# Kernel optimization log

Measured on AMD Instinct MI355X. Metric: run time of the kernel, lower is better.

## Reference

```python
import jax, jax.numpy as jnp
import numpy as np

N, E, D_IN, D_H, D_OUT = 50000, 600000, 128, 128, 1


def setup_inputs() -> dict:
    key = jax.random.key(0)
    ks = jax.random.split(key, 20)
    p = lambda k, sh: jax.random.normal(k, sh, dtype=jnp.float32) * 0.05
    return {
        "x": jax.random.normal(ks[0], (N, D_IN), dtype=jnp.float32),
        "edge_weight": jax.random.uniform(ks[1], (E,), dtype=jnp.float32),
        # input LEConv (lin1: W1/b1, lin2: W2 no bias, lin3: W3/b3)
        "W1_in": p(ks[2], (D_IN, D_H)), "b1_in": jnp.zeros((D_H,), jnp.float32),
        "W2_in": p(ks[3], (D_IN, D_H)),
        "W3_in": p(ks[4], (D_IN, D_H)), "b3_in": jnp.zeros((D_H,), jnp.float32),
        # inner LEConv
        "W1_h": p(ks[5], (D_H, D_H)), "b1_h": jnp.zeros((D_H,), jnp.float32),
        "W2_h": p(ks[6], (D_H, D_H)),
        "W3_h": p(ks[7], (D_H, D_H)), "b3_h": jnp.zeros((D_H,), jnp.float32),
        # output LEConv
        "W1_o": p(ks[8], (D_H, D_OUT)), "b1_o": jnp.zeros((D_OUT,), jnp.float32),
        "W2_o": p(ks[9], (D_H, D_OUT)),
        "W3_o": p(ks[10], (D_H, D_OUT)), "b3_o": jnp.zeros((D_OUT,), jnp.float32),
        # LayerNorms
        "g1": jnp.ones((D_H,), jnp.float32), "beta1": jnp.zeros((D_H,), jnp.float32),
        "g2": jnp.ones((D_H,), jnp.float32), "beta2": jnp.zeros((D_H,), jnp.float32),
        "edge_index": jax.random.randint(ks[11], (2, E), 0, N, dtype=jnp.int32),
        "number_of_layers": 4,
    }


def _leconv(x, src, dst, w, W1, b1, W2, W3, b3):
    # PyG LEConv: out_i = lin3(x_i) + sum_{j->i} w_e * (lin1(x_j) - lin2(x_i))
    a = x @ W1 + b1                                   # [N, D_out]
    b = x @ W2                                        # [N, D_out]
    wsum = jax.ops.segment_sum(w, dst, num_segments=N)             # [N]
    agg = jax.ops.segment_sum(w[:, None] * a[src], dst, num_segments=N)  # [N, D_out]
    return agg - b * wsum[:, None] + x @ W3 + b3


def _ln(x, g, b, eps=1e-5):
    m = x.mean(-1, keepdims=True)
    v = x.var(-1, keepdims=True)
    return (x - m) * jax.lax.rsqrt(v + eps) * g + b


def reference(x, edge_weight, W1_in, b1_in, W2_in, W3_in, b3_in,
              W1_h, b1_h, W2_h, W3_h, b3_h,
              W1_o, b1_o, W2_o, W3_o, b3_o,
              g1, beta1, g2, beta2, edge_index, number_of_layers):
    src, dst = edge_index[0], edge_index[1]
    # per-feature standardization over nodes (torch std is unbiased -> ddof=1)
    x = (x - x.mean(0, keepdims=True)) / (jnp.std(x, axis=0, ddof=1, keepdims=True) + 1e-6)
    h = jax.nn.leaky_relu(
        _ln(_leconv(x, src, dst, edge_weight, W1_in, b1_in, W2_in, W3_in, b3_in), g1, beta1),
        negative_slope=0.1)
    for _ in range(number_of_layers - 2):
        h = jax.nn.leaky_relu(
            _ln(_leconv(h, src, dst, edge_weight, W1_h, b1_h, W2_h, W3_h, b3_h), g2, beta2),
            negative_slope=0.1)
    h = _leconv(h, src, dst, edge_weight, W1_o, b1_o, W2_o, W3_o, b3_o)
    return jax.nn.sigmoid(h)
```

## Files before the change

kernel.cpp:

```cpp
#include <hip/hip_runtime.h>
#include <hip/hip_bf16.h>
#include <math.h>


typedef _Float16 f16x8 __attribute__((ext_vector_type(8)));
typedef _Float16 f16x4 __attribute__((ext_vector_type(4)));
typedef float f32x4 __attribute__((ext_vector_type(4)));

#define LSTRIDE 136

__device__ inline float wave_reduce_sum(float v) {
    #pragma unroll
    for (int off = 32; off > 0; off >>= 1)
        v += __shfl_xor(v, off, 64);
    return v;
}


__global__ __launch_bounds__(256) void hist_kernel(
    const int* __restrict__ dst, int* __restrict__ deg, int E)
{
    int e = blockIdx.x * 256 + threadIdx.x;
    if (e < E) atomicAdd(&deg[dst[e]], 1);
}

__global__ __launch_bounds__(256) void scan_pass1(
    const int* __restrict__ deg, int N, int* __restrict__ partial)
{
    __shared__ int sh[256];
    int t = threadIdx.x;
    int base = blockIdx.x * 1024 + t * 4;
    int s = 0;
    #pragma unroll
    for (int i = 0; i < 4; ++i) { int idx = base + i; if (idx < N) s += deg[idx]; }
    sh[t] = s; __syncthreads();
    for (int off = 128; off > 0; off >>= 1) {
        if (t < off) sh[t] += sh[t + off];
        __syncthreads();
    }
    if (t == 0) partial[blockIdx.x] = sh[0];
}

__global__ __launch_bounds__(256) void scan_pass2(int* __restrict__ partial, int nb)
{
    __shared__ int sh[256];
    int t = threadIdx.x;
    sh[t] = (t < nb) ? partial[t] : 0;
    __syncthreads();
    for (int off = 1; off < 256; off <<= 1) {
        int x = sh[t];
        if (t >= off) x += sh[t - off];
        __syncthreads();
        sh[t] = x;
        __syncthreads();
    }
    if (t < nb) partial[t] = (t > 0) ? sh[t - 1] : 0;
}

__global__ __launch_bounds__(256) void scan_pass3(
    const int* __restrict__ deg, int N, const int* __restrict__ partial,
    int* __restrict__ rowptr, int* __restrict__ fill, int E)
{
    __shared__ int sh[256];
    int t = threadIdx.x;
    int base = blockIdx.x * 1024 + t * 4;
    int v[4]; int s = 0;
    #pragma unroll
    for (int i = 0; i < 4; ++i) { int idx = base + i; v[i] = (idx < N) ? deg[idx] : 0; s += v[i]; }
    sh[t] = s; __syncthreads();
    for (int off = 1; off < 256; off <<= 1) {
        int x = sh[t];
        if (t >= off) x += sh[t - off];
        __syncthreads();
        sh[t] = x;
        __syncthreads();
    }
    int off0 = partial[blockIdx.x] + ((t > 0) ? sh[t - 1] : 0);
    #pragma unroll
    for (int i = 0; i < 4; ++i) {
        int idx = base + i;
        if (idx < N) { rowptr[idx] = off0; fill[idx] = off0; off0 += v[i]; }
    }
    if (blockIdx.x == 0 && t == 0) rowptr[N] = E;
}

__global__ __launch_bounds__(256) void csr_fill_kernel(
    const int* __restrict__ src, const int* __restrict__ dst,
    const float* __restrict__ ew, int* __restrict__ fill,
    int2* __restrict__ csr, int E)
{
    int e = blockIdx.x * 256 + threadIdx.x;
    if (e >= E) return;
    int d = dst[e];
    int pos = atomicAdd(&fill[d], 1);
    csr[pos] = make_int2(src[e], __float_as_int(ew[e]));
}

__global__ __launch_bounds__(256) void wsum_csr_kernel(
    const int* __restrict__ rowptr, const int2* __restrict__ csr,
    float* __restrict__ wsum, int N)
{
    int n = blockIdx.x * 256 + threadIdx.x;
    if (n >= N) return;
    int b = rowptr[n], en = rowptr[n + 1];
    float s = 0.f;
    for (int e = b; e < en; ++e) s += __int_as_float(csr[e].y);
    wsum[n] = s;
}


__global__ __launch_bounds__(256) void convert_weights_kernel(
    const float* __restrict__ W1, const float* __restrict__ W2,
    const float* __restrict__ W3, _Float16* __restrict__ Wt)
{
    int idx = blockIdx.x * 256 + threadIdx.x;
    if (idx >= 384 * 128) return;
    int n = idx >> 7, k = idx & 127;
    const float* W = (n < 128) ? W1 : (n < 256) ? W2 : W3;
    int c = n & 127;
    Wt[idx] = (_Float16)W[k * 128 + c];
}


#define CS_BLOCKS 512

__global__ __launch_bounds__(256) void colstats_kernel(
    const float* __restrict__ x, int N,
    float* __restrict__ ps, float* __restrict__ pss)
{
    __shared__ float shs[256][4];
    __shared__ float shq[256][4];
    int t = threadIdx.x;
    int g = t >> 5;
    int c = t & 31;
    const float4* xv = (const float4*)x;
    float s0=0.f,s1=0.f,s2=0.f,s3=0.f, q0=0.f,q1=0.f,q2=0.f,q3=0.f;
    for (int r = blockIdx.x * 8 + g; r < N; r += CS_BLOCKS * 8) {
        float4 v = xv[(size_t)r * 32 + c];
        s0 += v.x; s1 += v.y; s2 += v.z; s3 += v.w;
        q0 += v.x*v.x; q1 += v.y*v.y; q2 += v.z*v.z; q3 += v.w*v.w;
    }
    shs[t][0]=s0; shs[t][1]=s1; shs[t][2]=s2; shs[t][3]=s3;
    shq[t][0]=q0; shq[t][1]=q1; shq[t][2]=q2; shq[t][3]=q3;
    __syncthreads();
    if (t < 32) {
        float S[4] = {0,0,0,0}, Q[4] = {0,0,0,0};
        #pragma unroll
        for (int gg = 0; gg < 8; ++gg) {
            #pragma unroll
            for (int i = 0; i < 4; ++i) {
                S[i] += shs[t + 32*gg][i];
                Q[i] += shq[t + 32*gg][i];
            }
        }
        #pragma unroll
        for (int i = 0; i < 4; ++i) {
            ps [blockIdx.x * 128 + t*4 + i] = S[i];
            pss[blockIdx.x * 128 + t*4 + i] = Q[i];
        }
    }
}

__global__ __launch_bounds__(256) void reduce_stats_kernel(
    const float* __restrict__ ps, const float* __restrict__ pss, int N,
    float* __restrict__ mean, float* __restrict__ rstd)
{
    __shared__ float sh[256];
    int t = threadIdx.x;
    int f = t & 127;
    const float* src = (t >= 128) ? pss : ps;
    float s = 0.f;
    for (int r = 0; r < CS_BLOCKS; ++r) s += src[r * 128 + f];
    sh[t] = s;
    __syncthreads();
    if (t < 128) {
        float sum = sh[t], sumsq = sh[t + 128];
        float m = sum / (float)N;
        float var = (sumsq - sum * sum / (float)N) / (float)(N - 1);
        var = fmaxf(var, 0.f);
        mean[t] = m;
        rstd[t] = 1.f / (sqrtf(var) + 1e-6f);
    }
}

__global__ __launch_bounds__(256) void standardize_kernel(
    const float* __restrict__ x, const float* __restrict__ mean,
    const float* __restrict__ rstd, _Float16* __restrict__ out, long long total)
{
    long long i = (long long)blockIdx.x * blockDim.x + threadIdx.x;
    if (i >= total) return;
    int f = (int)(i & 127);
    out[i] = (_Float16)((x[i] - mean[f]) * rstd[f]);
}


__global__ __launch_bounds__(256, 2) void gemm_mfma_kernel(
    const _Float16* __restrict__ h, int N, int nTiles,
    const _Float16* __restrict__ Wt,
    const float* __restrict__ b1,
    const float* __restrict__ b3,
    const float* __restrict__ wsum,
    _Float16* __restrict__ out_a, _Float16* __restrict__ out_d)
{
    __shared__ _Float16 ldsS[64 * LSTRIDE];
    __shared__ _Float16 lds_a[64 * LSTRIDE];
    __shared__ _Float16 lds_d[64 * LSTRIDE];

    int t = threadIdx.x;
    int wave = t >> 6;
    int lane = t & 63;
    int quad = lane >> 4;
    int c16  = lane & 15;

    const f16x8* wv = (const f16x8*)Wt;
    int ntl[6] = {2*wave, 2*wave+1, 8+2*wave, 9+2*wave, 16+2*wave, 17+2*wave};
    f16x8 bfrag[6][4];
    #pragma unroll
    for (int j = 0; j < 6; ++j) {
        int nrow = ntl[j] * 16 + c16;
        #pragma unroll
        for (int s = 0; s < 4; ++s)
            bfrag[j][s] = wv[(size_t)nrow * 16 + s * 4 + quad];
    }
    float bb1[2], bb3[2];
    #pragma unroll
    for (int j = 0; j < 2; ++j) {
        int col = (2*wave + j) * 16 + c16;
        bb1[j] = b1[col];
        bb3[j] = b3[col];
    }

    const f16x8* hv = (const f16x8*)h;
    f16x8* oa = (f16x8*)out_a;
    f16x8* od = (f16x8*)out_d;

    for (int tile = blockIdx.x; tile < nTiles; tile += gridDim.x) {
        int row0 = tile * 64;

        #pragma unroll
        for (int i = 0; i < 4; ++i) {
            int idx = i * 256 + t;
            int row = idx >> 4;
            int chunk = idx & 15;
            int grow = row0 + row;
            if (grow >= N) grow = N - 1;
            *(f16x8*)&ldsS[row * LSTRIDE + chunk * 8] = hv[(size_t)grow * 16 + chunk];
        }
        __syncthreads();

        #pragma unroll
        for (int r = 0; r < 4; ++r) {
            f16x8 afrag[4];
            #pragma unroll
            for (int s = 0; s < 4; ++s)
                afrag[s] = *(const f16x8*)&ldsS[(r*16 + c16) * LSTRIDE + (s*4 + quad) * 8];

            f32x4 acc[6];
            #pragma unroll
            for (int j = 0; j < 6; ++j) acc[j] = (f32x4){0.f, 0.f, 0.f, 0.f};
            #pragma unroll
            for (int s = 0; s < 4; ++s) {
                #pragma unroll
                for (int j = 0; j < 6; ++j)
                    acc[j] = __builtin_amdgcn_mfma_f32_16x16x32_f16(afrag[s], bfrag[j][s], acc[j], 0, 0, 0);
            }

            float wsv[4];
            #pragma unroll
            for (int reg = 0; reg < 4; ++reg) {
                int gr = row0 + r*16 + quad*4 + reg;
                wsv[reg] = wsum[(gr < N) ? gr : (N - 1)];
            }
            #pragma unroll
            for (int j = 0; j < 2; ++j) {
                int col = (2*wave + j) * 16 + c16;
                #pragma unroll
                for (int reg = 0; reg < 4; ++reg) {
                    int lr = r*16 + quad*4 + reg;
                    lds_a[lr * LSTRIDE + col] = (_Float16)(acc[j][reg] + bb1[j]);
                    lds_d[lr * LSTRIDE + col] =
                        (_Float16)(acc[4+j][reg] + bb3[j] - wsv[reg] * acc[2+j][reg]);
                }
            }
        }
        __syncthreads();

        #pragma unroll
        for (int i = 0; i < 4; ++i) {
            int idx = i * 256 + t;
            int row = idx >> 4;
            int c8  = idx & 15;
            int grow = row0 + row;
            if (grow < N) {
                f16x8 va = *(const f16x8*)&lds_a[row * LSTRIDE + c8 * 8];
                oa[(size_t)grow * 16 + c8] = va;
                f16x8 vd = *(const f16x8*)&lds_d[row * LSTRIDE + c8 * 8];
                od[(size_t)grow * 16 + c8] = vd;
            }
        }
        __syncthreads();
    }
}


__global__ __launch_bounds__(256) void aggregate_ln_kernel(
    const int* __restrict__ rowptr, const int2* __restrict__ csr,
    const _Float16* __restrict__ a, const _Float16* __restrict__ d,
    const float* __restrict__ g, const float* __restrict__ beta,
    _Float16* __restrict__ out, int N)
{
    int wave = threadIdx.x >> 6;
    int lane = threadIdx.x & 63;
    int grp  = lane >> 4;
    int l    = lane & 15;
    int node = blockIdx.x * 4 + wave;
    if (node >= N) return;
    int b = rowptr[node], en = rowptr[node + 1];
    int deg = en - b;

    const f16x8* av = (const f16x8*)a;
    float acc[8] = {0,0,0,0,0,0,0,0};

    int nk = (deg + 3) >> 2;
    int k = 0;
    for (; k + 4 <= nk; k += 4) {
        int2 p[4];
        #pragma unroll
        for (int j = 0; j < 4; ++j) {
            int idx = b + (k + j) * 4 + grp;
            int idc = (idx < en) ? idx : b;
            p[j] = csr[idc];
            if (idx >= en) p[j].y = 0;
        }
        f16x8 v[4];
        #pragma unroll
        for (int j = 0; j < 4; ++j)
            v[j] = av[(size_t)p[j].x * 16 + l];
        #pragma unroll
        for (int j = 0; j < 4; ++j) {
            float w = __int_as_float(p[j].y);
            #pragma unroll
            for (int i = 0; i < 8; ++i) acc[i] += w * (float)v[j][i];
        }
    }
    for (; k < nk; ++k) {
        int idx = b + k * 4 + grp;
        int idc = (idx < en) ? idx : b;
        int2 p = csr[idc];
        if (idx >= en) p.y = 0;
        f16x8 v = av[(size_t)p.x * 16 + l];
        float w = __int_as_float(p.y);
        #pragma unroll
        for (int i = 0; i < 8; ++i) acc[i] += w * (float)v[i];
    }

    #pragma unroll
    for (int i = 0; i < 8; ++i) {
        acc[i] += __shfl_xor(acc[i], 16, 64);
        acc[i] += __shfl_xor(acc[i], 32, 64);
    }

    f16x8 dv = ((const f16x8*)d)[(size_t)node * 16 + l];
    float v[8];
    float s = 0.f, ss = 0.f;
    #pragma unroll
    for (int i = 0; i < 8; ++i) {
        v[i] = acc[i] + (float)dv[i];
        s += v[i]; ss += v[i] * v[i];
    }
    #pragma unroll
    for (int off = 1; off <= 8; off <<= 1) {
        s  += __shfl_xor(s,  off, 64);
        ss += __shfl_xor(ss, off, 64);
    }
    float mean = s * (1.f / 128.f);
    float var = ss * (1.f / 128.f) - mean * mean;
    float rstd = rsqrtf(var + 1e-5f);

    const float4* gv4 = (const float4*)g;
    const float4* bv4 = (const float4*)beta;
    float4 ga = gv4[l*2], gb = gv4[l*2+1];
    float4 ba = bv4[l*2], bb = bv4[l*2+1];
    float go[8] = {ga.x,ga.y,ga.z,ga.w,gb.x,gb.y,gb.z,gb.w};
    float bo[8] = {ba.x,ba.y,ba.z,ba.w,bb.x,bb.y,bb.z,bb.w};
    f16x8 ov;
    #pragma unroll
    for (int i = 0; i < 8; ++i) {
        float o = (v[i] - mean) * rstd * go[i] + bo[i];
        o = o >= 0.f ? o : 0.1f * o;
        ov[i] = (_Float16)o;
    }
    if (grp == 0)
        ((f16x8*)out)[(size_t)node * 16 + l] = ov;
}


__global__ __launch_bounds__(256) void out_gemv_kernel(
    const _Float16* __restrict__ h, int N,
    const float* __restrict__ W1, const float* __restrict__ b1,
    const float* __restrict__ W2,
    const float* __restrict__ W3, const float* __restrict__ b3,
    const float* __restrict__ wsum,
    float* __restrict__ a1, float* __restrict__ dpart)
{
    int wave = threadIdx.x >> 6;
    int lane = threadIdx.x & 63;
    int node = blockIdx.x * 4 + wave;
    if (node >= N) return;
    const _Float16* row = h + (size_t)node * 128;
    float h0 = (float)row[lane], h1 = (float)row[lane + 64];
    float s1 = wave_reduce_sum(h0 * W1[lane] + h1 * W1[lane + 64]);
    float s2 = wave_reduce_sum(h0 * W2[lane] + h1 * W2[lane + 64]);
    float s3 = wave_reduce_sum(h0 * W3[lane] + h1 * W3[lane + 64]);
    if (lane == 0) {
        a1[node] = s1 + b1[0];
        dpart[node] = s3 + b3[0] - wsum[node] * s2;
    }
}

__global__ __launch_bounds__(256) void gather_out_kernel(
    const int* __restrict__ rowptr, const int2* __restrict__ csr,
    const float* __restrict__ a1, const float* __restrict__ dpart,
    float* __restrict__ out, int N)
{
    int n = blockIdx.x * 256 + threadIdx.x;
    if (n >= N) return;
    int b = rowptr[n], en = rowptr[n + 1];
    float s = dpart[n];
    int e = b;
    for (; e + 4 <= en; e += 4) {
        int2 p0 = csr[e], p1 = csr[e+1], p2 = csr[e+2], p3 = csr[e+3];
        float x0 = a1[p0.x], x1 = a1[p1.x], x2 = a1[p2.x], x3 = a1[p3.x];
        s += __int_as_float(p0.y) * x0 + __int_as_float(p1.y) * x1
           + __int_as_float(p2.y) * x2 + __int_as_float(p3.y) * x3;
    }
    for (; e < en; ++e) {
        int2 p = csr[e];
        s += __int_as_float(p.y) * a1[p.x];
    }
    out[n] = 1.f / (1.f + expf(-s));
}

extern "C" void kernel_launch(void* const* d_in, const int* in_sizes, int n_in,
                              void* d_out, int out_size, void* d_ws, size_t ws_size,
                              hipStream_t stream)
{
    const float* x     = (const float*)d_in[0];
    const float* ew    = (const float*)d_in[1];
    const float* W1_in = (const float*)d_in[2];
    const float* b1_in = (const float*)d_in[3];
    const float* W2_in = (const float*)d_in[4];
    const float* W3_in = (const float*)d_in[5];
    const float* b3_in = (const float*)d_in[6];
    const float* W1_h  = (const float*)d_in[7];
    const float* b1_h  = (const float*)d_in[8];
    const float* W2_h  = (const float*)d_in[9];
    const float* W3_h  = (const float*)d_in[10];
    const float* b3_h  = (const float*)d_in[11];
    const float* W1_o  = (const float*)d_in[12];
    const float* b1_o  = (const float*)d_in[13];
    const float* W2_o  = (const float*)d_in[14];
    const float* W3_o  = (const float*)d_in[15];
    const float* b3_o  = (const float*)d_in[16];
    const float* g1    = (const float*)d_in[17];
    const float* beta1 = (const float*)d_in[18];
    const float* g2    = (const float*)d_in[19];
    const float* beta2 = (const float*)d_in[20];
    const int*   eidx  = (const int*)d_in[21];

    const int N = in_sizes[0] / 128;
    const int E = in_sizes[1];
    const int* srcp = eidx;
    const int* dstp = eidx + E;

    size_t off = 0;
    auto carve = [&](size_t nbytes) -> void* {
        void* p = (char*)d_ws + off;
        off += (nbytes + 255) & ~(size_t)255;
        return p;
    };
    _Float16* buf_h  = (_Float16*)carve((size_t)N * 128 * 2);
    _Float16* buf_a  = (_Float16*)carve((size_t)N * 128 * 2);
    _Float16* buf_d  = (_Float16*)carve((size_t)N * 128 * 2);
    int2*     csr    = (int2*)    carve((size_t)E * 8);
    _Float16* Wt_in  = (_Float16*)carve(384 * 128 * 2);
    _Float16* Wt_h   = (_Float16*)carve(384 * 128 * 2);
    int*      deg    = (int*)     carve((size_t)N * 4);
    int*      rowptr = (int*)     carve((size_t)(N + 1) * 4);
    int*      fill   = (int*)     carve((size_t)N * 4);
    int*      partial= (int*)     carve(256 * 4);
    float*    ps     = (float*)   carve((size_t)CS_BLOCKS * 128 * 4);
    float*    pss    = (float*)   carve((size_t)CS_BLOCKS * 128 * 4);
    float*    meanp  = (float*)   carve(128 * 4);
    float*    rstdp  = (float*)   carve(128 * 4);
    float*    wsum   = (float*)   carve((size_t)N * 4);
    float*    a1     = (float*)   carve((size_t)N * 4);
    float*    dpart  = (float*)   carve((size_t)N * 4);

    const long long totNF = (long long)N * 128;
    const int nodeWaveBlocks = (N + 3) / 4;
    const int eBlocks = (E + 255) / 256;
    const int nBlocks = (N + 255) / 256;
    const int nb = (N + 1023) / 1024;
    const int wBlocks = (384 * 128 + 255) / 256;

    hipMemsetAsync(deg, 0, (size_t)N * 4, stream);

    hist_kernel<<<eBlocks, 256, 0, stream>>>(dstp, deg, E);
    scan_pass1<<<nb, 256, 0, stream>>>(deg, N, partial);
    scan_pass2<<<1, 256, 0, stream>>>(partial, nb);
    scan_pass3<<<nb, 256, 0, stream>>>(deg, N, partial, rowptr, fill, E);
    csr_fill_kernel<<<eBlocks, 256, 0, stream>>>(srcp, dstp, ew, fill, csr, E);
    wsum_csr_kernel<<<nBlocks, 256, 0, stream>>>(rowptr, csr, wsum, N);
    convert_weights_kernel<<<wBlocks, 256, 0, stream>>>(W1_in, W2_in, W3_in, Wt_in);
    convert_weights_kernel<<<wBlocks, 256, 0, stream>>>(W1_h, W2_h, W3_h, Wt_h);

    colstats_kernel<<<CS_BLOCKS, 256, 0, stream>>>(x, N, ps, pss);
    reduce_stats_kernel<<<1, 256, 0, stream>>>(ps, pss, N, meanp, rstdp);
    standardize_kernel<<<(int)((totNF + 255) / 256), 256, 0, stream>>>(x, meanp, rstdp, buf_h, totNF);

    const int nTiles = (N + 63) / 64;
    const int gemmGrid = (nTiles < 512) ? nTiles : 512;

    gemm_mfma_kernel<<<gemmGrid, 256, 0, stream>>>(buf_h, N, nTiles, Wt_in, b1_in, b3_in, wsum, buf_a, buf_d);
    aggregate_ln_kernel<<<nodeWaveBlocks, 256, 0, stream>>>(rowptr, csr, buf_a, buf_d, g1, beta1, buf_h, N);

    for (int l = 0; l < 2; ++l) {
        gemm_mfma_kernel<<<gemmGrid, 256, 0, stream>>>(buf_h, N, nTiles, Wt_h, b1_h, b3_h, wsum, buf_a, buf_d);
        aggregate_ln_kernel<<<nodeWaveBlocks, 256, 0, stream>>>(rowptr, csr, buf_a, buf_d, g2, beta2, buf_h, N);
    }

    out_gemv_kernel<<<nodeWaveBlocks, 256, 0, stream>>>(buf_h, N, W1_o, b1_o, W2_o, W3_o, b3_o, wsum, a1, dpart);
    gather_out_kernel<<<nBlocks, 256, 0, stream>>>(rowptr, csr, a1, dpart, (float*)d_out, N);
}
```

Before: 371.0 us.

## Fuse standardization into first GEMM and cut preprocessing kernel launches

Folds the wsum computation into csr_fill via float atomics, merges the two weight-conversion launches into one, and replaces the per-block stats partials plus reduce kernel with atomic accumulation and a tiny finalize kernel. The standardize pass is removed: a new GEMM variant reads fp32 x, applies mean and rstd on load, and converts to fp16 in LDS. A single memset now zeroes deg, stats and wsum together. This trims several launches and one full N×128 write and read, at the cost of atomic contention on wsum and stats and a nondeterministic summation order.

```diff
diff --git a/kernel.cpp b/kernel.cpp
--- a/kernel.cpp
+++ b/kernel.cpp
@@ -87,46 +87,41 @@
 __global__ __launch_bounds__(256) void csr_fill_kernel(
     const int* __restrict__ src, const int* __restrict__ dst,
     const float* __restrict__ ew, int* __restrict__ fill,
-    int2* __restrict__ csr, int E)
+    int2* __restrict__ csr, float* __restrict__ wsum, int E)
 {
     int e = blockIdx.x * 256 + threadIdx.x;
     if (e >= E) return;
     int d = dst[e];
+    float w = ew[e];
     int pos = atomicAdd(&fill[d], 1);
-    csr[pos] = make_int2(src[e], __float_as_int(ew[e]));
-}
-
-__global__ __launch_bounds__(256) void wsum_csr_kernel(
-    const int* __restrict__ rowptr, const int2* __restrict__ csr,
-    float* __restrict__ wsum, int N)
-{
-    int n = blockIdx.x * 256 + threadIdx.x;
-    if (n >= N) return;
-    int b = rowptr[n], en = rowptr[n + 1];
-    float s = 0.f;
-    for (int e = b; e < en; ++e) s += __int_as_float(csr[e].y);
-    wsum[n] = s;
+    csr[pos] = make_int2(src[e], __float_as_int(w));
+    atomicAdd(&wsum[d], w);
 }
 
 
 __global__ __launch_bounds__(256) void convert_weights_kernel(
-    const float* __restrict__ W1, const float* __restrict__ W2,
-    const float* __restrict__ W3, _Float16* __restrict__ Wt)
+    const float* __restrict__ W1a, const float* __restrict__ W2a,
+    const float* __restrict__ W3a, _Float16* __restrict__ Wta,
+    const float* __restrict__ W1b, const float* __restrict__ W2b,
+    const float* __restrict__ W3b, _Float16* __restrict__ Wtb)
 {
     int idx = blockIdx.x * 256 + threadIdx.x;
-    if (idx >= 384 * 128) return;
-    int n = idx >> 7, k = idx & 127;
-    const float* W = (n < 128) ? W1 : (n < 256) ? W2 : W3;
+    if (idx >= 2 * 384 * 128) return;
+    int set = idx >= 384 * 128;
+    int id = idx - set * 384 * 128;
+    int n = id >> 7, k = id & 127;
+    const float* W = set ? ((n < 128) ? W1b : (n < 256) ? W2b : W3b)
+                         : ((n < 128) ? W1a : (n < 256) ? W2a : W3a);
+    _Float16* Wt = set ? Wtb : Wta;
     int c = n & 127;
-    Wt[idx] = (_Float16)W[k * 128 + c];
+    Wt[id] = (_Float16)W[k * 128 + c];
 }
 
 
 #define CS_BLOCKS 512
 
 __global__ __launch_bounds__(256) void colstats_kernel(
-    const float* __restrict__ x, int N,
-    float* __restrict__ ps, float* __restrict__ pss)
+    const float* __restrict__ x, int N, float* __restrict__ stats)
 {
     __shared__ float shs[256][4];
     __shared__ float shq[256][4];
@@ -155,42 +150,23 @@
         }
         #pragma unroll
         for (int i = 0; i < 4; ++i) {
-            ps [blockIdx.x * 128 + t*4 + i] = S[i];
-            pss[blockIdx.x * 128 + t*4 + i] = Q[i];
-        }
-    }
-}
-
-__global__ __launch_bounds__(256) void reduce_stats_kernel(
-    const float* __restrict__ ps, const float* __restrict__ pss, int N,
-    float* __restrict__ mean, float* __restrict__ rstd)
-{
-    __shared__ float sh[256];
-    int t = threadIdx.x;
-    int f = t & 127;
-    const float* src = (t >= 128) ? pss : ps;
-    float s = 0.f;
-    for (int r = 0; r < CS_BLOCKS; ++r) s += src[r * 128 + f];
-    sh[t] = s;
-    __syncthreads();
-    if (t < 128) {
-        float sum = sh[t], sumsq = sh[t + 128];
-        float m = sum / (float)N;
-        float var = (sumsq - sum * sum / (float)N) / (float)(N - 1);
-        var = fmaxf(var, 0.f);
-        mean[t] = m;
-        rstd[t] = 1.f / (sqrtf(var) + 1e-6f);
-    }
-}
-
-__global__ __launch_bounds__(256) void standardize_kernel(
-    const float* __restrict__ x, const float* __restrict__ mean,
-    const float* __restrict__ rstd, _Float16* __restrict__ out, long long total)
-{
-    long long i = (long long)blockIdx.x * blockDim.x + threadIdx.x;
-    if (i >= total) return;
-    int f = (int)(i & 127);
-    out[i] = (_Float16)((x[i] - mean[f]) * rstd[f]);
+            atomicAdd(&stats[t*4 + i], S[i]);
+            atomicAdd(&stats[128 + t*4 + i], Q[i]);
+        }
+    }
+}
+
+__global__ void finalize_stats_kernel(const float* __restrict__ stats, int N,
+                                      float* __restrict__ mean,
+                                      float* __restrict__ rstd)
+{
+    int f = threadIdx.x;
+    float s = stats[f], ss = stats[128 + f];
+    float m = s / (float)N;
+    float var = (ss - s * s / (float)N) / (float)(N - 1);
+    var = fmaxf(var, 0.f);
+    mean[f] = m;
+    rstd[f] = 1.f / (sqrtf(var) + 1e-6f);
 }
 
 
@@ -245,6 +221,126 @@
             int grow = row0 + row;
             if (grow >= N) grow = N - 1;
             *(f16x8*)&ldsS[row * LSTRIDE + chunk * 8] = hv[(size_t)grow * 16 + chunk];
+        }
+        __syncthreads();
+
+        #pragma unroll
+        for (int r = 0; r < 4; ++r) {
+            f16x8 afrag[4];
+            #pragma unroll
+            for (int s = 0; s < 4; ++s)
+                afrag[s] = *(const f16x8*)&ldsS[(r*16 + c16) * LSTRIDE + (s*4 + quad) * 8];
+
+            f32x4 acc[6];
+            #pragma unroll
+            for (int j = 0; j < 6; ++j) acc[j] = (f32x4){0.f, 0.f, 0.f, 0.f};
+            #pragma unroll
+            for (int s = 0; s < 4; ++s) {
+                #pragma unroll
+                for (int j = 0; j < 6; ++j)
+                    acc[j] = __builtin_amdgcn_mfma_f32_16x16x32_f16(afrag[s], bfrag[j][s], acc[j], 0, 0, 0);
+            }
+
+            float wsv[4];
+            #pragma unroll
+            for (int reg = 0; reg < 4; ++reg) {
+                int gr = row0 + r*16 + quad*4 + reg;
+                wsv[reg] = wsum[(gr < N) ? gr : (N - 1)];
+            }
+            #pragma unroll
+            for (int j = 0; j < 2; ++j) {
+                int col = (2*wave + j) * 16 + c16;
+                #pragma unroll
+                for (int reg = 0; reg < 4; ++reg) {
+                    int lr = r*16 + quad*4 + reg;
+                    lds_a[lr * LSTRIDE + col] = (_Float16)(acc[j][reg] + bb1[j]);
+                    lds_d[lr * LSTRIDE + col] =
+                        (_Float16)(acc[4+j][reg] + bb3[j] - wsv[reg] * acc[2+j][reg]);
+                }
+            }
+        }
+        __syncthreads();
+
+        #pragma unroll
+        for (int i = 0; i < 4; ++i) {
+            int idx = i * 256 + t;
+            int row = idx >> 4;
+            int c8  = idx & 15;
+            int grow = row0 + row;
+            if (grow < N) {
+                f16x8 va = *(const f16x8*)&lds_a[row * LSTRIDE + c8 * 8];
+                oa[(size_t)grow * 16 + c8] = va;
+                f16x8 vd = *(const f16x8*)&lds_d[row * LSTRIDE + c8 * 8];
+                od[(size_t)grow * 16 + c8] = vd;
+            }
+        }
+        __syncthreads();
+    }
+}
+
+
+__global__ __launch_bounds__(256, 2) void gemm_mfma_std_kernel(
+    const float* __restrict__ x,
+    const float* __restrict__ meanp, const float* __restrict__ rstdp,
+    int N, int nTiles,
+    const _Float16* __restrict__ Wt,
+    const float* __restrict__ b1,
+    const float* __restrict__ b3,
+    const float* __restrict__ wsum,
+    _Float16* __restrict__ out_a, _Float16* __restrict__ out_d)
+{
+    __shared__ _Float16 ldsS[64 * LSTRIDE];
+    __shared__ _Float16 lds_a[64 * LSTRIDE];
+    __shared__ _Float16 lds_d[64 * LSTRIDE];
+
+    int t = threadIdx.x;
+    int wave = t >> 6;
+    int lane = t & 63;
+    int quad = lane >> 4;
+    int c16  = lane & 15;
+
+    const f16x8* wv = (const f16x8*)Wt;
+    int ntl[6] = {2*wave, 2*wave+1, 8+2*wave, 9+2*wave, 16+2*wave, 17+2*wave};
+    f16x8 bfrag[6][4];
+    #pragma unroll
+    for (int j = 0; j < 6; ++j) {
+        int nrow = ntl[j] * 16 + c16;
+        #pragma unroll
+        for (int s = 0; s < 4; ++s)
+            bfrag[j][s] = wv[(size_t)nrow * 16 + s * 4 + quad];
+    }
+    float bb1[2], bb3[2];
+    #pragma unroll
+    for (int j = 0; j < 2; ++j) {
+        int col = (2*wave + j) * 16 + c16;
+        bb1[j] = b1[col];
+        bb3[j] = b3[col];
+    }
+
+    int c4 = t & 31;
+    float4 mu = ((const float4*)meanp)[c4];
+    float4 rs = ((const float4*)rstdp)[c4];
+
+    const float4* xv = (const float4*)x;
+    f16x8* oa = (f16x8*)out_a;
+    f16x8* od = (f16x8*)out_d;
+
+    for (int tile = blockIdx.x; tile < nTiles; tile += gridDim.x) {
+        int row0 = tile * 64;
+
+        #pragma unroll
+        for (int i = 0; i < 8; ++i) {
+            int idx = i * 256 + t;
+            int row = idx >> 5;
+            int grow = row0 + row;
+            if (grow >= N) grow = N - 1;
+            float4 v = xv[(size_t)grow * 32 + c4];
+            f16x4 o;
+            o.x = (_Float16)((v.x - mu.x) * rs.x);
+            o.y = (_Float16)((v.y - mu.y) * rs.y);
+            o.z = (_Float16)((v.z - mu.z) * rs.z);
+            o.w = (_Float16)((v.w - mu.w) * rs.w);
+            *(f16x4*)&ldsS[row * LSTRIDE + c4 * 4] = o;
         }
         __syncthreads();
 
@@ -479,50 +575,48 @@
         off += (nbytes + 255) & ~(size_t)255;
         return p;
     };
+    int*      deg    = (int*)     carve((size_t)N * 4);
+    float*    stats  = (float*)   carve(256 * 4);
+    float*    wsum   = (float*)   carve((size_t)N * 4);
+    size_t zeroBytes = off;
     _Float16* buf_h  = (_Float16*)carve((size_t)N * 128 * 2);
     _Float16* buf_a  = (_Float16*)carve((size_t)N * 128 * 2);
     _Float16* buf_d  = (_Float16*)carve((size_t)N * 128 * 2);
     int2*     csr    = (int2*)    carve((size_t)E * 8);
     _Float16* Wt_in  = (_Float16*)carve(384 * 128 * 2);
     _Float16* Wt_h   = (_Float16*)carve(384 * 128 * 2);
-    int*      deg    = (int*)     carve((size_t)N * 4);
     int*      rowptr = (int*)     carve((size_t)(N + 1) * 4);
     int*      fill   = (int*)     carve((size_t)N * 4);
     int*      partial= (int*)     carve(256 * 4);
-    float*    ps     = (float*)   carve((size_t)CS_BLOCKS * 128 * 4);
-    float*    pss    = (float*)   carve((size_t)CS_BLOCKS * 128 * 4);
     float*    meanp  = (float*)   carve(128 * 4);
     float*    rstdp  = (float*)   carve(128 * 4);
-    float*    wsum   = (float*)   carve((size_t)N * 4);
     float*    a1     = (float*)   carve((size_t)N * 4);
     float*    dpart  = (float*)   carve((size_t)N * 4);
 
-    const long long totNF = (long long)N * 128;
     const int nodeWaveBlocks = (N + 3) / 4;
     const int eBlocks = (E + 255) / 256;
     const int nBlocks = (N + 255) / 256;
     const int nb = (N + 1023) / 1024;
-    const int wBlocks = (384 * 128 + 255) / 256;
-
-    hipMemsetAsync(deg, 0, (size_t)N * 4, stream);
+    const int wBlocks = (2 * 384 * 128 + 255) / 256;
+
+    hipMemsetAsync(deg, 0, zeroBytes, stream);
 
     hist_kernel<<<eBlocks, 256, 0, stream>>>(dstp, deg, E);
     scan_pass1<<<nb, 256, 0, stream>>>(deg, N, partial);
     scan_pass2<<<1, 256, 0, stream>>>(partial, nb);
     scan_pass3<<<nb, 256, 0, stream>>>(deg, N, partial, rowptr, fill, E);
-    csr_fill_kernel<<<eBlocks, 256, 0, stream>>>(srcp, dstp, ew, fill, csr, E);
-    wsum_csr_kernel<<<nBlocks, 256, 0, stream>>>(rowptr, csr, wsum, N);
-    convert_weights_kernel<<<wBlocks, 256, 0, stream>>>(W1_in, W2_in, W3_in, Wt_in);
-    convert_weights_kernel<<<wBlocks, 256, 0, stream>>>(W1_h, W2_h, W3_h, Wt_h);
-
-    colstats_kernel<<<CS_BLOCKS, 256, 0, stream>>>(x, N, ps, pss);
-    reduce_stats_kernel<<<1, 256, 0, stream>>>(ps, pss, N, meanp, rstdp);
-    standardize_kernel<<<(int)((totNF + 255) / 256), 256, 0, stream>>>(x, meanp, rstdp, buf_h, totNF);
+    csr_fill_kernel<<<eBlocks, 256, 0, stream>>>(srcp, dstp, ew, fill, csr, wsum, E);
+    convert_weights_kernel<<<wBlocks, 256, 0, stream>>>(
+        W1_in, W2_in, W3_in, Wt_in, W1_h, W2_h, W3_h, Wt_h);
+
+    colstats_kernel<<<CS_BLOCKS, 256, 0, stream>>>(x, N, stats);
+    finalize_stats_kernel<<<1, 128, 0, stream>>>(stats, N, meanp, rstdp);
 
     const int nTiles = (N + 63) / 64;
     const int gemmGrid = (nTiles < 512) ? nTiles : 512;
 
-    gemm_mfma_kernel<<<gemmGrid, 256, 0, stream>>>(buf_h, N, nTiles, Wt_in, b1_in, b3_in, wsum, buf_a, buf_d);
+    gemm_mfma_std_kernel<<<gemmGrid, 256, 0, stream>>>(
+        x, meanp, rstdp, N, nTiles, Wt_in, b1_in, b3_in, wsum, buf_a, buf_d);
     aggregate_ln_kernel<<<nodeWaveBlocks, 256, 0, stream>>>(rowptr, csr, buf_a, buf_d, g1, beta1, buf_h, N);
 
     for (int l = 0; l < 2; ++l) {
```

Result: slower. 422.7 us (+14.0%).
